# Optimization experiments

Measured on AMD Instinct MI355X. Metric: run time of the kernel, lower is better.

## Reference

```python
import jax, jax.numpy as jnp
import numpy as np

EPS = 1e-5

def conv2d(x, w, stride=1, pad=0, groups=1):
    return jax.lax.conv_general_dilated(
        x, w, (stride, stride), [(pad, pad), (pad, pad)],
        feature_group_count=groups,
        dimension_numbers=('NCHW', 'OIHW', 'NCHW'))

def prelu(x, a):
    return jnp.where(x > 0, x, a[None, :, None, None] * x)

def batchnorm(x, g, b):
    # training-mode BN: batch statistics over N,H,W (biased variance, as torch)
    m = jnp.mean(x, axis=(0, 2, 3), keepdims=True)
    v = jnp.var(x, axis=(0, 2, 3), keepdims=True)
    xhat = (x - m) * jax.lax.rsqrt(v + EPS)
    return xhat * g[None, :, None, None] + b[None, :, None, None]

def setup_inputs() -> dict:
    key = jax.random.key(0)
    ks = jax.random.split(key, 8)
    C_in, C_out, stride = 128, 256, 2
    x = jax.random.normal(ks[0], (32, C_in, 56, 56), dtype=jnp.float32)
    w1 = jax.random.normal(ks[1], (C_out, C_in, 1, 1), dtype=jnp.float32) * 0.05
    w_dw = jax.random.normal(ks[2], (C_out, 1, 3, 3), dtype=jnp.float32) * 0.1
    w3 = jax.random.normal(ks[3], (C_out, C_out, 1, 1), dtype=jnp.float32) * 0.05
    w_adj = jax.random.normal(ks[4], (C_out, C_in, 1, 1), dtype=jnp.float32) * 0.05
    a_init = jnp.full((C_out,), 0.25, dtype=jnp.float32)  # PReLU init
    ones = jnp.ones((C_out,), dtype=jnp.float32)
    zeros = jnp.zeros((C_out,), dtype=jnp.float32)
    return {
        'x': x,
        'w1': w1, 'a1': a_init, 'g1': ones, 'b1': zeros,
        'w_dw': w_dw, 'a2': a_init, 'g2': ones, 'b2': zeros,
        'w3': w3, 'a3': a_init, 'g3': ones, 'b3': zeros,
        'w_adj': w_adj,
    }

def reference(x, w1, a1, g1, b1, w_dw, a2, g2, b2, w3, a3, g3, b3, w_adj):
    stride, C_out = 2, w_dw.shape[0]
    residual = conv2d(x, w_adj, stride=stride)  # full-precision shortcut
    xs = jnp.sign(x)
    # binary 1x1 conv (sign(x) already signed; sign is idempotent)
    out = conv2d(jnp.sign(xs), jnp.sign(w1))
    out = batchnorm(prelu(out, a1), g1, b1)
    # binary depthwise 3x3, stride, pad 1
    out = conv2d(jnp.sign(out), jnp.sign(w_dw), stride=stride, pad=1, groups=C_out)
    out = batchnorm(prelu(out, a2), g2, b2)
    # binary 1x1 conv
    out = conv2d(jnp.sign(out), jnp.sign(w3))
    out = batchnorm(prelu(out, a3), g3, b3)
    return out + residual
```

## Files before the change

### kernel.cpp

```cpp
#include <hip/hip_runtime.h>
#include <stdint.h>

#define NB   32
#define CIN  128
#define COUT 256
#define HH   56
#define WW   56
#define S1   (HH*WW)
#define HO   28
#define WO   28
#define S2   (HO*WO)
#define NS1  (NB*S1)
#define NS2  (NB*S2)
#define TOT2 (NS2*COUT)
#define EPSV 1e-5f

constexpr size_t OFF_XBITS = 0;
constexpr size_t OFF_WB1   = OFF_XBITS + (size_t)NS1*8*4;
constexpr size_t OFF_WB3   = OFF_WB1 + 256*8*4;
constexpr size_t OFF_WDW   = OFF_WB3 + 256*16*4;
constexpr size_t OFF_ACC   = OFF_WDW + 4096;
constexpr size_t OFF_WBADJ = OFF_ACC + 3*256*4*sizeof(int);
constexpr size_t OFF_XG    = OFF_WBADJ + (size_t)COUT*CIN*2;
constexpr size_t OFF_OUT1  = OFF_XG + (size_t)NS2*CIN*2;
constexpr size_t OFF_OUT2  = OFF_OUT1 + (size_t)NS1*COUT;
constexpr size_t OFF_XB2   = OFF_OUT2 + (size_t)TOT2;
constexpr size_t OFF_OUT3  = OFF_XB2 + (size_t)NS2*16*4;

typedef __attribute__((ext_vector_type(8))) short bf16x8;
typedef __attribute__((ext_vector_type(4))) float f32x4;

__device__ __forceinline__ uint32_t f2bf(float v) {
  uint32_t u = __float_as_uint(v);
  return (u + 0x7fffu + ((u >> 16) & 1u)) >> 16;
}

__device__ __forceinline__ void bn_finalize(const int* __restrict__ acc4,
                                            float a, float g, float b, float inv_ns,
                                            float& sc, float& sh) {
  float ps = (float)acc4[0];
  float ng = (float)acc4[1];
  float pq = (float)acc4[2];
  float nq = (float)acc4[3];
  float mean = (ps + a*ng) * inv_ns;
  float ex2  = (pq + a*a*nq) * inv_ns;
  float var  = ex2 - mean*mean;
  float rs   = rsqrtf(var + EPSV);
  sc = rs * g;
  sh = b - mean * sc;
}

__global__ __launch_bounds__(256) void packx_kernel(
    const float* __restrict__ x, uint32_t* __restrict__ xbits,
    uint32_t* __restrict__ xg,
    const float* __restrict__ w1, const float* __restrict__ w3,
    const float* __restrict__ wdw, const float* __restrict__ wadj,
    uint32_t* __restrict__ wb1, uint32_t* __restrict__ wb3,
    int8_t* __restrict__ wdws, uint32_t* __restrict__ wbadj,
    int* __restrict__ accbase) {
  int wdx = blockIdx.y;
  if (wdx == 0 && blockIdx.x < 256 && threadIdx.x < 64) {
    int co = blockIdx.x;
    int l  = threadIdx.x;
    if (l < 12) {
      int set = l >> 2, k = l & 3;
      accbase[set*1024 + co*4 + k] = 0;
    }
    for (int h = 0; h < 2; ++h) {
      float v = w1[(size_t)co*CIN + h*64 + l];
      unsigned long long bp = __ballot(v > 0.f);
      unsigned long long bn = __ballot(v < 0.f);
      if (l == 0) {
        wb1[co*8 + 2*h    ] = (uint32_t)bp;
        wb1[co*8 + 2*h + 1] = (uint32_t)(bp >> 32);
        wb1[co*8 + 4 + 2*h    ] = (uint32_t)bn;
        wb1[co*8 + 4 + 2*h + 1] = (uint32_t)(bn >> 32);
      }
    }
    for (int h = 0; h < 4; ++h) {
      float v = w3[(size_t)co*COUT + h*64 + l];
      unsigned long long bp = __ballot(v > 0.f);
      unsigned long long bn = __ballot(v < 0.f);
      if (l == 0) {
        wb3[co*16 + 2*h    ] = (uint32_t)bp;
        wb3[co*16 + 2*h + 1] = (uint32_t)(bp >> 32);
        wb3[co*16 + 8 + 2*h    ] = (uint32_t)bn;
        wb3[co*16 + 8 + 2*h + 1] = (uint32_t)(bn >> 32);
      }
    }
    if (l < 9) {
      float v = wdw[co*9 + l];
      wdws[co*9 + l] = (int8_t)((v > 0.f) - (v < 0.f));
    }
    {
      float v0 = wadj[(size_t)co*CIN + 2*l];
      float v1 = wadj[(size_t)co*CIN + 2*l + 1];
      wbadj[co*64 + l] = f2bf(v0) | (f2bf(v1) << 16);
    }
  }

  int m = blockIdx.x*256 + threadIdx.x;
  int n = m / S1, hw = m % S1;
  size_t base = ((size_t)n*CIN + wdx*32)*S1 + hw;
  uint32_t p = 0, q = 0;
  uint32_t bv[16];
  #pragma unroll
  for (int j = 0; j < 32; ++j) {
    float v = x[base + (size_t)j*S1];
    p |= (uint32_t)(v > 0.f) << j;
    q |= (uint32_t)(v < 0.f) << j;
    uint32_t b = f2bf(v);
    if (j & 1) bv[j >> 1] |= b << 16; else bv[j >> 1] = b;
  }
  xbits[(size_t)m*8 + wdx    ] = p;
  xbits[(size_t)m*8 + 4 + wdx] = q;
  int h = hw / WW, w = hw % WW;
  if (((h | w) & 1) == 0) {
    int m2 = n*S2 + (h >> 1)*WO + (w >> 1);
    uint4* dst = (uint4*)(xg + (size_t)m2*64 + wdx*16);
    dst[0] = make_uint4(bv[0],  bv[1],  bv[2],  bv[3]);
    dst[1] = make_uint4(bv[4],  bv[5],  bv[6],  bv[7]);
    dst[2] = make_uint4(bv[8],  bv[9],  bv[10], bv[11]);
    dst[3] = make_uint4(bv[12], bv[13], bv[14], bv[15]);
  }
}

__global__ __launch_bounds__(256) void conv1_kernel(
    const uint32_t* __restrict__ xb, const uint32_t* __restrict__ wb,
    int8_t* __restrict__ out1) {
  int m = blockIdx.x*256 + threadIdx.x;
  int n = m / S1, hw = m % S1;
  const uint32_t* xw = xb + (size_t)m*8;
  uint32_t p0 = xw[0], p1 = xw[1], p2 = xw[2], p3 = xw[3];
  uint32_t q0 = xw[4], q1 = xw[5], q2 = xw[6], q3 = xw[7];
  int co0 = blockIdx.y * 32;
  size_t obase = ((size_t)n*COUT)*S1 + hw;
  bool nozero = (((p0|q0) & (p1|q1) & (p2|q2) & (p3|q3)) == 0xffffffffu);
  if (nozero) {
    #pragma unroll 4
    for (int co = co0; co < co0 + 32; ++co) {
      const uint32_t* w8 = wb + (size_t)co*8;
      int s = __popc(p0 ^ w8[0]) + __popc(p1 ^ w8[1])
            + __popc(p2 ^ w8[2]) + __popc(p3 ^ w8[3]);
      int acc = 128 - 2*s;
      if (acc > 127) acc = 127;
      out1[obase + (size_t)co*S1] = (int8_t)acc;
    }
  } else {
    #pragma unroll 4
    for (int co = co0; co < co0 + 32; ++co) {
      const uint32_t* w8 = wb + (size_t)co*8;
      uint32_t a0 = w8[0], a1 = w8[1], a2 = w8[2], a3 = w8[3];
      uint32_t b0 = w8[4], b1 = w8[5], b2 = w8[6], b3 = w8[7];
      int acc = __popc(p0&a0) + __popc(p1&a1) + __popc(p2&a2) + __popc(p3&a3)
              + __popc(q0&b0) + __popc(q1&b1) + __popc(q2&b2) + __popc(q3&b3)
              - __popc(p0&b0) - __popc(p1&b1) - __popc(p2&b2) - __popc(p3&b3)
              - __popc(q0&a0) - __popc(q1&a1) - __popc(q2&a2) - __popc(q3&a3);
      if (acc > 127) acc = 127;
      out1[obase + (size_t)co*S1] = (int8_t)acc;
    }
  }
}

__global__ __launch_bounds__(256) void stats_i8_kernel(
    const int8_t* __restrict__ buf, int* __restrict__ accum,
    int s_sp, int v16_per_block) {
  int co = blockIdx.x, slice = blockIdx.y;
  int base16 = slice * v16_per_block;
  int psum = 0, nsum = 0, psq = 0, nsq = 0;
  for (int i = threadIdx.x; i < v16_per_block; i += 256) {
    int flat = (base16 + i) * 16;
    int n = flat / s_sp, hw = flat % s_sp;
    int4 v = *reinterpret_cast<const int4*>(buf + (size_t)(n*COUT + co)*s_sp + hw);
    int ws[4] = {v.x, v.y, v.z, v.w};
    #pragma unroll
    for (int d = 0; d < 4; ++d) {
      #pragma unroll
      for (int k = 0; k < 4; ++k) {
        int f = (int)(int8_t)(ws[d] >> (8*k));
        if (f > 0) { psum += f; psq += f*f; } else { nsum += f; nsq += f*f; }
      }
    }
  }
  __shared__ int r0[256], r1[256], r2[256], r3[256];
  int t = threadIdx.x;
  r0[t] = psum; r1[t] = nsum; r2[t] = psq; r3[t] = nsq;
  __syncthreads();
  for (int s = 128; s > 0; s >>= 1) {
    if (t < s) { r0[t]+=r0[t+s]; r1[t]+=r1[t+s]; r2[t]+=r2[t+s]; r3[t]+=r3[t+s]; }
    __syncthreads();
  }
  if (t == 0) {
    atomicAdd(&accum[co*4+0], r0[0]);
    atomicAdd(&accum[co*4+1], r1[0]);
    atomicAdd(&accum[co*4+2], r2[0]);
    atomicAdd(&accum[co*4+3], r3[0]);
  }
}

__global__ __launch_bounds__(256) void stats_i16_kernel(
    const int16_t* __restrict__ buf, int* __restrict__ accum,
    int s_sp, int v8_per_block) {
  int co = blockIdx.x, slice = blockIdx.y;
  int base8 = slice * v8_per_block;
  int psum = 0, nsum = 0, psq = 0, nsq = 0;
  for (int i = threadIdx.x; i < v8_per_block; i += 256) {
    int flat = (base8 + i) * 8;
    int n = flat / s_sp, hw = flat % s_sp;
    int4 v = *reinterpret_cast<const int4*>(buf + (size_t)(n*COUT + co)*s_sp + hw);
    int ws[4] = {v.x, v.y, v.z, v.w};
    #pragma unroll
    for (int d = 0; d < 4; ++d) {
      int lo = (int)(short)(ws[d] & 0xffff);
      int hi = (int)(short)(ws[d] >> 16);
      if (lo > 0) { psum += lo; psq += lo*lo; } else { nsum += lo; nsq += lo*lo; }
      if (hi > 0) { psum += hi; psq += hi*hi; } else { nsum += hi; nsq += hi*hi; }
    }
  }
  __shared__ int r0[256], r1[256], r2[256], r3[256];
  int t = threadIdx.x;
  r0[t] = psum; r1[t] = nsum; r2[t] = psq; r3[t] = nsq;
  __syncthreads();
  for (int s = 128; s > 0; s >>= 1) {
    if (t < s) { r0[t]+=r0[t+s]; r1[t]+=r1[t+s]; r2[t]+=r2[t+s]; r3[t]+=r3[t+s]; }
    __syncthreads();
  }
  if (t == 0) {
    atomicAdd(&accum[co*4+0], r0[0]);
    atomicAdd(&accum[co*4+1], r1[0]);
    atomicAdd(&accum[co*4+2], r2[0]);
    atomicAdd(&accum[co*4+3], r3[0]);
  }
}

#define DW_SLABS 8
#define DW_RB    68
__global__ __launch_bounds__(256) void dw_kernel(
    const int8_t* __restrict__ out1, const int8_t* __restrict__ wdws,
    const int* __restrict__ acc1, const float* __restrict__ a1,
    const float* __restrict__ g1, const float* __restrict__ b1,
    int8_t* __restrict__ out2, int* __restrict__ accum2) {
  __shared__ int8_t sl[DW_SLABS][57][DW_RB];
  __shared__ int sTp[DW_SLABS], sTn[DW_SLABS], sAcc[DW_SLABS][4];
  int tid = threadIdx.x;
  int nc0 = blockIdx.x * DW_SLABS;
  int co0 = nc0 & (COUT-1);

  int* slw = (int*)&sl[0][0][0];
  #pragma unroll
  for (int i = tid; i < DW_SLABS*57*DW_RB/4; i += 256) slw[i] = 0;
  if (tid < DW_SLABS) { sTp[tid] = 128; sTn[tid] = -129; }
  if (tid < DW_SLABS*4) sAcc[tid >> 2][tid & 3] = 0;
  __syncthreads();

  {
    int slab = tid >> 5;
    int co = co0 + slab;
    float av = a1[co], sc, sh;
    bn_finalize(acc1 + co*4, av, g1[co], b1[co], 1.f/NS1, sc, sh);
    int tp = 128, tn = -129;
    int v0 = -128 + (tid & 31)*8;
    #pragma unroll
    for (int k = 0; k < 8; ++k) {
      int v = v0 + k;
      float f = (float)v;
      float pr = f > 0.f ? f : av*f;
      float tv = pr*sc + sh;
      if (tv > 0.f && v < tp) tp = v;
      if (tv < 0.f && v > tn) tn = v;
    }
    atomicMin(&sTp[slab], tp);
    atomicMax(&sTn[slab], tn);
  }
  __syncthreads();

  for (int i = tid; i < DW_SLABS*784; i += 256) {
    int slab = i / 784;
    int d    = i - slab*784;
    int ih   = d / 14;
    int iwd  = d - ih*14;
    int Tp = sTp[slab], Tn = sTn[slab];
    uint32_t v4 = ((const uint32_t*)(out1 + (size_t)(nc0 + slab)*S1))[d];
    uint32_t s4 = 0;
    #pragma unroll
    for (int k = 0; k < 4; ++k) {
      int v = (int)(int8_t)(v4 >> (8*k));
      int s = (v >= Tp) - (v <= Tn);
      s4 |= (uint32_t)(s & 0xff) << (8*k);
    }
    *(uint32_t*)&sl[slab][ih + 1][4 + 4*iwd] = s4;
  }
  __syncthreads();

  int psum = 0, nsum = 0, psq = 0, nsq = 0;
  int slabD = tid / HO;
  if (tid < DW_SLABS*HO) {
    int ho   = tid - slabD*HO;
    int nc = nc0 + slabD;
    int co = co0 + slabD;
    int wv[9];
    #pragma unroll
    for (int k = 0; k < 9; ++k) wv[k] = wdws[co*9 + k];
    const uint32_t* r0 = (const uint32_t*)&sl[slabD][2*ho    ][4];
    const uint32_t* r1 = (const uint32_t*)&sl[slabD][2*ho + 1][4];
    const uint32_t* r2 = (const uint32_t*)&sl[slabD][2*ho + 2][4];
    uint32_t* o32 = (uint32_t*)(out2 + (size_t)nc*S2 + ho*WO);
    int c0 = 0, c1 = 0, c2 = 0;
    uint32_t obuf = 0;
    #pragma unroll
    for (int q = 0; q < 14; ++q) {
      uint32_t d0 = r0[q], d1 = r1[q], d2 = r2[q];
      int s00=(int)(int8_t)d0, s01=(int)(int8_t)(d0>>8), s02=(int)(int8_t)(d0>>16), s03=(int)(int8_t)(d0>>24);
      int s10=(int)(int8_t)d1, s11=(int)(int8_t)(d1>>8), s12=(int)(int8_t)(d1>>16), s13=(int)(int8_t)(d1>>24);
      int s20=(int)(int8_t)d2, s21=(int)(int8_t)(d2>>8), s22=(int)(int8_t)(d2>>16), s23=(int)(int8_t)(d2>>24);
      int a0 = c0*wv[0] + s00*wv[1] + s01*wv[2]
             + c1*wv[3] + s10*wv[4] + s11*wv[5]
             + c2*wv[6] + s20*wv[7] + s21*wv[8];
      int a1v = s01*wv[0] + s02*wv[1] + s03*wv[2]
              + s11*wv[3] + s12*wv[4] + s13*wv[5]
              + s21*wv[6] + s22*wv[7] + s23*wv[8];
      c0 = s03; c1 = s13; c2 = s23;
      if (a0 > 0) { psum += a0; psq += a0*a0; } else { nsum += a0; nsq += a0*a0; }
      if (a1v > 0) { psum += a1v; psq += a1v*a1v; } else { nsum += a1v; nsq += a1v*a1v; }
      if ((q & 1) == 0) {
        obuf = (uint32_t)(a0 & 0xff) | ((uint32_t)(a1v & 0xff) << 8);
      } else {
        obuf |= ((uint32_t)(a0 & 0xff) << 16) | ((uint32_t)(a1v & 0xff) << 24);
        o32[q >> 1] = obuf;
      }
    }
    atomicAdd(&sAcc[slabD][0], psum);
    atomicAdd(&sAcc[slabD][1], nsum);
    atomicAdd(&sAcc[slabD][2], psq);
    atomicAdd(&sAcc[slabD][3], nsq);
  }
  __syncthreads();

  if (tid < DW_SLABS*4) {
    int slab = tid >> 2, k = tid & 3;
    atomicAdd(&accum2[(co0 + slab)*4 + k], sAcc[slab][k]);
  }
}

__global__ __launch_bounds__(256) void pack2_kernel(
    const int8_t* __restrict__ out2, const int* __restrict__ acc2,
    const float* __restrict__ a2, const float* __restrict__ g2,
    const float* __restrict__ b2, uint32_t* __restrict__ xb2) {
  __shared__ int sTp[32], sTn[32];
  int wdx = blockIdx.y;
  if (threadIdx.x < 32) {
    int c = wdx*32 + threadIdx.x;
    float av = a2[c], sc, sh;
    bn_finalize(acc2 + c*4, av, g2[c], b2[c], 1.f/NS2, sc, sh);
    int tp = 10, tn = -10;
    for (int v = -9; v <= 9; ++v) {
      float f = (float)v;
      float pr = f > 0.f ? f : av*f;
      float tv = pr*sc + sh;
      if (tv > 0.f && v < tp) tp = v;
      if (tv < 0.f && v > tn) tn = v;
    }
    sTp[threadIdx.x] = tp; sTn[threadIdx.x] = tn;
  }
  __syncthreads();
  int m = blockIdx.x*256 + threadIdx.x;
  int n = m / S2, hw = m % S2;
  uint32_t p = 0, q = 0;
  #pragma unroll
  for (int j = 0; j < 32; ++j) {
    int c = wdx*32 + j;
    int v = out2[(size_t)(n*COUT + c)*S2 + hw];
    p |= (uint32_t)(v >= sTp[j]) << j;
    q |= (uint32_t)(v <= sTn[j]) << j;
  }
  xb2[(size_t)m*16 + wdx    ] = p;
  xb2[(size_t)m*16 + 8 + wdx] = q;
}

__global__ __launch_bounds__(256) void conv3_kernel(
    const uint32_t* __restrict__ xb2, const uint32_t* __restrict__ wb3,
    int16_t* __restrict__ out3) {
  int m = blockIdx.x*256 + threadIdx.x;
  int n = m / S2, hw = m % S2;
  const uint32_t* xw = xb2 + (size_t)m*16;
  uint32_t P[8], Q[8];
  #pragma unroll
  for (int i = 0; i < 8; ++i) { P[i] = xw[i]; Q[i] = xw[8+i]; }
  int co0 = blockIdx.y * 32;
  size_t obase = ((size_t)n*COUT)*S2 + hw;
  uint32_t allm = 0xffffffffu;
  #pragma unroll
  for (int i = 0; i < 8; ++i) allm &= (P[i] | Q[i]);
  if (allm == 0xffffffffu) {
    #pragma unroll 2
    for (int co = co0; co < co0 + 32; ++co) {
      const uint32_t* w = wb3 + (size_t)co*16;
      int s = 0;
      #pragma unroll
      for (int i = 0; i < 8; ++i) s += __popc(P[i] ^ w[i]);
      out3[obase + (size_t)co*S2] = (int16_t)(256 - 2*s);
    }
  } else {
    #pragma unroll 2
    for (int co = co0; co < co0 + 32; ++co) {
      const uint32_t* w = wb3 + (size_t)co*16;
      int acc = 0;
      #pragma unroll
      for (int i = 0; i < 8; ++i) {
        uint32_t wp = w[i], wn = w[8+i];
        acc += __popc(P[i]&wp) + __popc(Q[i]&wn) - __popc(P[i]&wn) - __popc(Q[i]&wp);
      }
      out3[obase + (size_t)co*S2] = (int16_t)acc;
    }
  }
}

__global__ __launch_bounds__(256) void resfinal_kernel(
    const uint16_t* __restrict__ xg, const uint16_t* __restrict__ wb,
    const int16_t* __restrict__ out3,
    const float* __restrict__ a3, const float* __restrict__ g3,
    const float* __restrict__ b3, const int* __restrict__ acc3,
    float* __restrict__ out) {
  int lane = threadIdx.x & 63;
  int wid  = threadIdx.x >> 6;
  int m0  = blockIdx.x*64 + wid*16;
  int co0 = blockIdx.y*64;
  int r16 = lane & 15, hi = lane >> 4;
  int koff = hi * 8;

  const bf16x8* arow = (const bf16x8*)(xg + (size_t)(m0 + r16)*CIN + koff);
  bf16x8 af0 = arow[0], af1 = arow[4], af2 = arow[8], af3 = arow[12];

  f32x4 d0, d1, d2, d3;
  {
    const bf16x8* brow = (const bf16x8*)(wb + (size_t)(co0 + r16)*CIN + koff);
    f32x4 a = {0.f,0.f,0.f,0.f};
    a = __builtin_amdgcn_mfma_f32_16x16x32_bf16(af0, brow[0],  a, 0,0,0);
    a = __builtin_amdgcn_mfma_f32_16x16x32_bf16(af1, brow[4],  a, 0,0,0);
    a = __builtin_amdgcn_mfma_f32_16x16x32_bf16(af2, brow[8],  a, 0,0,0);
    a = __builtin_amdgcn_mfma_f32_16x16x32_bf16(af3, brow[12], a, 0,0,0);
    d0 = a;
  }
  {
    const bf16x8* brow = (const bf16x8*)(wb + (size_t)(co0 + 16 + r16)*CIN + koff);
    f32x4 a = {0.f,0.f,0.f,0.f};
    a = __builtin_amdgcn_mfma_f32_16x16x32_bf16(af0, brow[0],  a, 0,0,0);
    a = __builtin_amdgcn_mfma_f32_16x16x32_bf16(af1, brow[4],  a, 0,0,0);
    a = __builtin_amdgcn_mfma_f32_16x16x32_bf16(af2, brow[8],  a, 0,0,0);
    a = __builtin_amdgcn_mfma_f32_16x16x32_bf16(af3, brow[12], a, 0,0,0);
    d1 = a;
  }
  {
    const bf16x8* brow = (const bf16x8*)(wb + (size_t)(co0 + 32 + r16)*CIN + koff);
    f32x4 a = {0.f,0.f,0.f,0.f};
    a = __builtin_amdgcn_mfma_f32_16x16x32_bf16(af0, brow[0],  a, 0,0,0);
    a = __builtin_amdgcn_mfma_f32_16x16x32_bf16(af1, brow[4],  a, 0,0,0);
    a = __builtin_amdgcn_mfma_f32_16x16x32_bf16(af2, brow[8],  a, 0,0,0);
    a = __builtin_amdgcn_mfma_f32_16x16x32_bf16(af3, brow[12], a, 0,0,0);
    d2 = a;
  }
  {
    const bf16x8* brow = (const bf16x8*)(wb + (size_t)(co0 + 48 + r16)*CIN + koff);
    f32x4 a = {0.f,0.f,0.f,0.f};
    a = __builtin_amdgcn_mfma_f32_16x16x32_bf16(af0, brow[0],  a, 0,0,0);
    a = __builtin_amdgcn_mfma_f32_16x16x32_bf16(af1, brow[4],  a, 0,0,0);
    a = __builtin_amdgcn_mfma_f32_16x16x32_bf16(af2, brow[8],  a, 0,0,0);
    a = __builtin_amdgcn_mfma_f32_16x16x32_bf16(af3, brow[12], a, 0,0,0);
    d3 = a;
  }

  int mrow = m0 + hi*4;
  int n  = mrow / S2;
  int hw = mrow - n*S2;
  f32x4 dd[4] = {d0, d1, d2, d3};
  #pragma unroll
  for (int t = 0; t < 4; ++t) {
    int co = co0 + t*16 + r16;
    float av = a3[co], sc, sh;
    bn_finalize(acc3 + co*4, av, g3[co], b3[co], 1.f/NS2, sc, sh);
    size_t o = ((size_t)n*COUT + co)*S2 + hw;
    #pragma unroll
    for (int r = 0; r < 4; ++r) {
      float f = (float)out3[o + r];
      float pp = f > 0.f ? f : av*f;
      out[o + r] = pp*sc + sh + dd[t][r];
    }
  }
}

extern "C" void kernel_launch(void* const* d_in, const int* in_sizes, int n_in,
                              void* d_out, int out_size, void* d_ws, size_t ws_size,
                              hipStream_t stream) {
  (void)in_sizes; (void)n_in; (void)out_size; (void)ws_size;
  const float* x    = (const float*)d_in[0];
  const float* w1   = (const float*)d_in[1];
  const float* a1   = (const float*)d_in[2];
  const float* g1   = (const float*)d_in[3];
  const float* b1   = (const float*)d_in[4];
  const float* wdw  = (const float*)d_in[5];
  const float* a2   = (const float*)d_in[6];
  const float* g2   = (const float*)d_in[7];
  const float* b2   = (const float*)d_in[8];
  const float* w3   = (const float*)d_in[9];
  const float* a3   = (const float*)d_in[10];
  const float* g3   = (const float*)d_in[11];
  const float* b3   = (const float*)d_in[12];
  const float* wadj = (const float*)d_in[13];
  float* out = (float*)d_out;

  char* ws = (char*)d_ws;
  uint32_t* xbits = (uint32_t*)(ws + OFF_XBITS);
  uint32_t* wb1   = (uint32_t*)(ws + OFF_WB1);
  uint32_t* wb3   = (uint32_t*)(ws + OFF_WB3);
  int8_t*   wdws  = (int8_t*)  (ws + OFF_WDW);
  int*      acc1  = (int*)     (ws + OFF_ACC);
  int*      acc2  = acc1 + 256*4;
  int*      acc3  = acc2 + 256*4;
  uint32_t* wbadj = (uint32_t*)(ws + OFF_WBADJ);
  uint32_t* xg    = (uint32_t*)(ws + OFF_XG);
  int8_t*   out1  = (int8_t*)  (ws + OFF_OUT1);
  int8_t*   out2  = (int8_t*)  (ws + OFF_OUT2);
  uint32_t* xb2   = (uint32_t*)(ws + OFF_XB2);
  int16_t*  out3  = (int16_t*) (ws + OFF_OUT3);

  packx_kernel<<<dim3(NS1/256, 4), 256, 0, stream>>>(
      x, xbits, xg, w1, w3, wdw, wadj, wb1, wb3, wdws, wbadj, acc1);
  conv1_kernel<<<dim3(NS1/256, 8), 256, 0, stream>>>(xbits, wb1, out1);
  stats_i8_kernel<<<dim3(256, 4), 256, 0, stream>>>(out1, acc1, S1, 1568);
  dw_kernel<<<NB*COUT/DW_SLABS, 256, 0, stream>>>(out1, wdws, acc1, a1, g1, b1, out2, acc2);
  pack2_kernel<<<dim3(NS2/256, 8), 256, 0, stream>>>(out2, acc2, a2, g2, b2, xb2);
  conv3_kernel<<<dim3(NS2/256, 8), 256, 0, stream>>>(xb2, wb3, out3);
  stats_i16_kernel<<<dim3(256, 4), 256, 0, stream>>>(out3, acc3, S2, 784);
  resfinal_kernel<<<dim3(NS2/64, COUT/64), 256, 0, stream>>>(
      (const uint16_t*)xg, (const uint16_t*)wbadj, out3, a3, g3, b3, acc3, out);
}
```

Measured before the change: 110.0 us.

## Fuse BN statistics into conv1 and conv3 and widen resfinal blocks

The separate int8 and int16 BN-statistics kernels are removed. conv1 and conv3 now keep their 32 per-thread outputs in registers, transpose them through shared memory, reduce per-channel positive and negative sums and squares with shuffles, and atomically add them to the accumulators. This avoids re-reading out1 and out3 from global memory and saves two launches, at the cost of many more atomics (one set per block per channel). resfinal now computes all 256 output channels per block with 16 MFMA tiles instead of 64, which raises register pressure but reuses the A fragments and cuts the grid size.

```diff
diff --git a/kernel.cpp b/kernel.cpp
--- a/kernel.cpp
+++ b/kernel.cpp
@@ -127,29 +127,31 @@
 
 __global__ __launch_bounds__(256) void conv1_kernel(
     const uint32_t* __restrict__ xb, const uint32_t* __restrict__ wb,
-    int8_t* __restrict__ out1) {
-  int m = blockIdx.x*256 + threadIdx.x;
+    int8_t* __restrict__ out1, int* __restrict__ accum1) {
+  int tid = threadIdx.x;
+  int m = blockIdx.x*256 + tid;
   int n = m / S1, hw = m % S1;
   const uint32_t* xw = xb + (size_t)m*8;
   uint32_t p0 = xw[0], p1 = xw[1], p2 = xw[2], p3 = xw[3];
   uint32_t q0 = xw[4], q1 = xw[5], q2 = xw[6], q3 = xw[7];
   int co0 = blockIdx.y * 32;
   size_t obase = ((size_t)n*COUT)*S1 + hw;
+  int8_t a8[32];
   bool nozero = (((p0|q0) & (p1|q1) & (p2|q2) & (p3|q3)) == 0xffffffffu);
   if (nozero) {
     #pragma unroll 4
-    for (int co = co0; co < co0 + 32; ++co) {
-      const uint32_t* w8 = wb + (size_t)co*8;
+    for (int j = 0; j < 32; ++j) {
+      const uint32_t* w8 = wb + (size_t)(co0 + j)*8;
       int s = __popc(p0 ^ w8[0]) + __popc(p1 ^ w8[1])
             + __popc(p2 ^ w8[2]) + __popc(p3 ^ w8[3]);
       int acc = 128 - 2*s;
       if (acc > 127) acc = 127;
-      out1[obase + (size_t)co*S1] = (int8_t)acc;
+      a8[j] = (int8_t)acc;
     }
   } else {
     #pragma unroll 4
-    for (int co = co0; co < co0 + 32; ++co) {
-      const uint32_t* w8 = wb + (size_t)co*8;
+    for (int j = 0; j < 32; ++j) {
+      const uint32_t* w8 = wb + (size_t)(co0 + j)*8;
       uint32_t a0 = w8[0], a1 = w8[1], a2 = w8[2], a3 = w8[3];
       uint32_t b0 = w8[4], b1 = w8[5], b2 = w8[6], b3 = w8[7];
       int acc = __popc(p0&a0) + __popc(p1&a1) + __popc(p2&a2) + __popc(p3&a3)
@@ -157,79 +159,42 @@
               - __popc(p0&b0) - __popc(p1&b1) - __popc(p2&b2) - __popc(p3&b3)
               - __popc(q0&a0) - __popc(q1&a1) - __popc(q2&a2) - __popc(q3&a3);
       if (acc > 127) acc = 127;
-      out1[obase + (size_t)co*S1] = (int8_t)acc;
-    }
-  }
-}
-
-__global__ __launch_bounds__(256) void stats_i8_kernel(
-    const int8_t* __restrict__ buf, int* __restrict__ accum,
-    int s_sp, int v16_per_block) {
-  int co = blockIdx.x, slice = blockIdx.y;
-  int base16 = slice * v16_per_block;
-  int psum = 0, nsum = 0, psq = 0, nsq = 0;
-  for (int i = threadIdx.x; i < v16_per_block; i += 256) {
-    int flat = (base16 + i) * 16;
-    int n = flat / s_sp, hw = flat % s_sp;
-    int4 v = *reinterpret_cast<const int4*>(buf + (size_t)(n*COUT + co)*s_sp + hw);
-    int ws[4] = {v.x, v.y, v.z, v.w};
-    #pragma unroll
-    for (int d = 0; d < 4; ++d) {
-      #pragma unroll
-      for (int k = 0; k < 4; ++k) {
-        int f = (int)(int8_t)(ws[d] >> (8*k));
-        if (f > 0) { psum += f; psq += f*f; } else { nsum += f; nsq += f*f; }
-      }
-    }
-  }
-  __shared__ int r0[256], r1[256], r2[256], r3[256];
-  int t = threadIdx.x;
-  r0[t] = psum; r1[t] = nsum; r2[t] = psq; r3[t] = nsq;
-  __syncthreads();
-  for (int s = 128; s > 0; s >>= 1) {
-    if (t < s) { r0[t]+=r0[t+s]; r1[t]+=r1[t+s]; r2[t]+=r2[t+s]; r3[t]+=r3[t+s]; }
-    __syncthreads();
-  }
-  if (t == 0) {
-    atomicAdd(&accum[co*4+0], r0[0]);
-    atomicAdd(&accum[co*4+1], r1[0]);
-    atomicAdd(&accum[co*4+2], r2[0]);
-    atomicAdd(&accum[co*4+3], r3[0]);
-  }
-}
-
-__global__ __launch_bounds__(256) void stats_i16_kernel(
-    const int16_t* __restrict__ buf, int* __restrict__ accum,
-    int s_sp, int v8_per_block) {
-  int co = blockIdx.x, slice = blockIdx.y;
-  int base8 = slice * v8_per_block;
-  int psum = 0, nsum = 0, psq = 0, nsq = 0;
-  for (int i = threadIdx.x; i < v8_per_block; i += 256) {
-    int flat = (base8 + i) * 8;
-    int n = flat / s_sp, hw = flat % s_sp;
-    int4 v = *reinterpret_cast<const int4*>(buf + (size_t)(n*COUT + co)*s_sp + hw);
-    int ws[4] = {v.x, v.y, v.z, v.w};
-    #pragma unroll
-    for (int d = 0; d < 4; ++d) {
-      int lo = (int)(short)(ws[d] & 0xffff);
-      int hi = (int)(short)(ws[d] >> 16);
-      if (lo > 0) { psum += lo; psq += lo*lo; } else { nsum += lo; nsq += lo*lo; }
-      if (hi > 0) { psum += hi; psq += hi*hi; } else { nsum += hi; nsq += hi*hi; }
-    }
-  }
-  __shared__ int r0[256], r1[256], r2[256], r3[256];
-  int t = threadIdx.x;
-  r0[t] = psum; r1[t] = nsum; r2[t] = psq; r3[t] = nsq;
-  __syncthreads();
-  for (int s = 128; s > 0; s >>= 1) {
-    if (t < s) { r0[t]+=r0[t+s]; r1[t]+=r1[t+s]; r2[t]+=r2[t+s]; r3[t]+=r3[t+s]; }
-    __syncthreads();
-  }
-  if (t == 0) {
-    atomicAdd(&accum[co*4+0], r0[0]);
-    atomicAdd(&accum[co*4+1], r1[0]);
-    atomicAdd(&accum[co*4+2], r2[0]);
-    atomicAdd(&accum[co*4+3], r3[0]);
+      a8[j] = (int8_t)acc;
+    }
+  }
+  #pragma unroll 8
+  for (int j = 0; j < 32; ++j) out1[obase + (size_t)(co0 + j)*S1] = a8[j];
+
+  __shared__ int8_t vals[256][36];
+  #pragma unroll
+  for (int k = 0; k < 8; ++k) {
+    uint32_t w4 = (uint32_t)(uint8_t)a8[4*k]
+                | ((uint32_t)(uint8_t)a8[4*k+1] << 8)
+                | ((uint32_t)(uint8_t)a8[4*k+2] << 16)
+                | ((uint32_t)(uint8_t)a8[4*k+3] << 24);
+    *(uint32_t*)&vals[tid][4*k] = w4;
+  }
+  __syncthreads();
+  int j = tid >> 3;
+  int c = tid & 7;
+  int ps = 0, ns = 0, pq = 0, nq = 0;
+  #pragma unroll
+  for (int i = 0; i < 32; ++i) {
+    int v = (int)vals[c*32 + i][j];
+    if (v > 0) { ps += v; pq += v*v; } else { ns += v; nq += v*v; }
+  }
+  #pragma unroll
+  for (int off = 4; off; off >>= 1) {
+    ps += __shfl_xor(ps, off);
+    ns += __shfl_xor(ns, off);
+    pq += __shfl_xor(pq, off);
+    nq += __shfl_xor(nq, off);
+  }
+  if (c == 0) {
+    atomicAdd(&accum1[(co0 + j)*4 + 0], ps);
+    atomicAdd(&accum1[(co0 + j)*4 + 1], ns);
+    atomicAdd(&accum1[(co0 + j)*4 + 2], pq);
+    atomicAdd(&accum1[(co0 + j)*4 + 3], nq);
   }
 }
 
@@ -379,8 +344,9 @@
 
 __global__ __launch_bounds__(256) void conv3_kernel(
     const uint32_t* __restrict__ xb2, const uint32_t* __restrict__ wb3,
-    int16_t* __restrict__ out3) {
-  int m = blockIdx.x*256 + threadIdx.x;
+    int16_t* __restrict__ out3, int* __restrict__ accum3) {
+  int tid = threadIdx.x;
+  int m = blockIdx.x*256 + tid;
   int n = m / S2, hw = m % S2;
   const uint32_t* xw = xb2 + (size_t)m*16;
   uint32_t P[8], Q[8];
@@ -388,30 +354,62 @@
   for (int i = 0; i < 8; ++i) { P[i] = xw[i]; Q[i] = xw[8+i]; }
   int co0 = blockIdx.y * 32;
   size_t obase = ((size_t)n*COUT)*S2 + hw;
+  int16_t a16[32];
   uint32_t allm = 0xffffffffu;
   #pragma unroll
   for (int i = 0; i < 8; ++i) allm &= (P[i] | Q[i]);
   if (allm == 0xffffffffu) {
     #pragma unroll 2
-    for (int co = co0; co < co0 + 32; ++co) {
-      const uint32_t* w = wb3 + (size_t)co*16;
+    for (int j = 0; j < 32; ++j) {
+      const uint32_t* w = wb3 + (size_t)(co0 + j)*16;
       int s = 0;
       #pragma unroll
       for (int i = 0; i < 8; ++i) s += __popc(P[i] ^ w[i]);
-      out3[obase + (size_t)co*S2] = (int16_t)(256 - 2*s);
+      a16[j] = (int16_t)(256 - 2*s);
     }
   } else {
     #pragma unroll 2
-    for (int co = co0; co < co0 + 32; ++co) {
-      const uint32_t* w = wb3 + (size_t)co*16;
+    for (int j = 0; j < 32; ++j) {
+      const uint32_t* w = wb3 + (size_t)(co0 + j)*16;
       int acc = 0;
       #pragma unroll
       for (int i = 0; i < 8; ++i) {
         uint32_t wp = w[i], wn = w[8+i];
         acc += __popc(P[i]&wp) + __popc(Q[i]&wn) - __popc(P[i]&wn) - __popc(Q[i]&wp);
       }
-      out3[obase + (size_t)co*S2] = (int16_t)acc;
-    }
+      a16[j] = (int16_t)acc;
+    }
+  }
+  #pragma unroll 8
+  for (int j = 0; j < 32; ++j) out3[obase + (size_t)(co0 + j)*S2] = a16[j];
+
+  __shared__ int16_t vals[256][34];
+  #pragma unroll
+  for (int k = 0; k < 16; ++k) {
+    uint32_t w2 = (uint32_t)(uint16_t)a16[2*k] | ((uint32_t)(uint16_t)a16[2*k+1] << 16);
+    *(uint32_t*)&vals[tid][2*k] = w2;
+  }
+  __syncthreads();
+  int j = tid >> 3;
+  int c = tid & 7;
+  int ps = 0, ns = 0, pq = 0, nq = 0;
+  #pragma unroll
+  for (int i = 0; i < 32; ++i) {
+    int v = (int)vals[c*32 + i][j];
+    if (v > 0) { ps += v; pq += v*v; } else { ns += v; nq += v*v; }
+  }
+  #pragma unroll
+  for (int off = 4; off; off >>= 1) {
+    ps += __shfl_xor(ps, off);
+    ns += __shfl_xor(ns, off);
+    pq += __shfl_xor(pq, off);
+    nq += __shfl_xor(nq, off);
+  }
+  if (c == 0) {
+    atomicAdd(&accum3[(co0 + j)*4 + 0], ps);
+    atomicAdd(&accum3[(co0 + j)*4 + 1], ns);
+    atomicAdd(&accum3[(co0 + j)*4 + 2], pq);
+    atomicAdd(&accum3[(co0 + j)*4 + 3], nq);
   }
 }
 
@@ -424,58 +422,30 @@
   int lane = threadIdx.x & 63;
   int wid  = threadIdx.x >> 6;
   int m0  = blockIdx.x*64 + wid*16;
-  int co0 = blockIdx.y*64;
   int r16 = lane & 15, hi = lane >> 4;
   int koff = hi * 8;
 
   const bf16x8* arow = (const bf16x8*)(xg + (size_t)(m0 + r16)*CIN + koff);
   bf16x8 af0 = arow[0], af1 = arow[4], af2 = arow[8], af3 = arow[12];
 
-  f32x4 d0, d1, d2, d3;
-  {
-    const bf16x8* brow = (const bf16x8*)(wb + (size_t)(co0 + r16)*CIN + koff);
+  f32x4 dd[16];
+  #pragma unroll
+  for (int t = 0; t < 16; ++t) {
+    const bf16x8* brow = (const bf16x8*)(wb + (size_t)(t*16 + r16)*CIN + koff);
     f32x4 a = {0.f,0.f,0.f,0.f};
     a = __builtin_amdgcn_mfma_f32_16x16x32_bf16(af0, brow[0],  a, 0,0,0);
     a = __builtin_amdgcn_mfma_f32_16x16x32_bf16(af1, brow[4],  a, 0,0,0);
     a = __builtin_amdgcn_mfma_f32_16x16x32_bf16(af2, brow[8],  a, 0,0,0);
     a = __builtin_amdgcn_mfma_f32_16x16x32_bf16(af3, brow[12], a, 0,0,0);
-    d0 = a;
-  }
-  {
-    const bf16x8* brow = (const bf16x8*)(wb + (size_t)(co0 + 16 + r16)*CIN + koff);
-    f32x4 a = {0.f,0.f,0.f,0.f};
-    a = __builtin_amdgcn_mfma_f32_16x16x32_bf16(af0, brow[0],  a, 0,0,0);
-    a = __builtin_amdgcn_mfma_f32_16x16x32_bf16(af1, brow[4],  a, 0,0,0);
-    a = __builtin_amdgcn_mfma_f32_16x16x32_bf16(af2, brow[8],  a, 0,0,0);
-    a = __builtin_amdgcn_mfma_f32_16x16x32_bf16(af3, brow[12], a, 0,0,0);
-    d1 = a;
-  }
-  {
-    const bf16x8* brow = (const bf16x8*)(wb + (size_t)(co0 + 32 + r16)*CIN + koff);
-    f32x4 a = {0.f,0.f,0.f,0.f};
-    a = __builtin_amdgcn_mfma_f32_16x16x32_bf16(af0, brow[0],  a, 0,0,0);
-    a = __builtin_amdgcn_mfma_f32_16x16x32_bf16(af1, brow[4],  a, 0,0,0);
-    a = __builtin_amdgcn_mfma_f32_16x16x32_bf16(af2, brow[8],  a, 0,0,0);
-    a = __builtin_amdgcn_mfma_f32_16x16x32_bf16(af3, brow[12], a, 0,0,0);
-    d2 = a;
-  }
-  {
-    const bf16x8* brow = (const bf16x8*)(wb + (size_t)(co0 + 48 + r16)*CIN + koff);
-    f32x4 a = {0.f,0.f,0.f,0.f};
-    a = __builtin_amdgcn_mfma_f32_16x16x32_bf16(af0, brow[0],  a, 0,0,0);
-    a = __builtin_amdgcn_mfma_f32_16x16x32_bf16(af1, brow[4],  a, 0,0,0);
-    a = __builtin_amdgcn_mfma_f32_16x16x32_bf16(af2, brow[8],  a, 0,0,0);
-    a = __builtin_amdgcn_mfma_f32_16x16x32_bf16(af3, brow[12], a, 0,0,0);
-    d3 = a;
+    dd[t] = a;
   }
 
   int mrow = m0 + hi*4;
   int n  = mrow / S2;
   int hw = mrow - n*S2;
-  f32x4 dd[4] = {d0, d1, d2, d3};
-  #pragma unroll
-  for (int t = 0; t < 4; ++t) {
-    int co = co0 + t*16 + r16;
+  #pragma unroll
+  for (int t = 0; t < 16; ++t) {
+    int co = t*16 + r16;
     float av = a3[co], sc, sh;
     bn_finalize(acc3 + co*4, av, g3[co], b3[co], 1.f/NS2, sc, sh);
     size_t o = ((size_t)n*COUT + co)*S2 + hw;
@@ -525,12 +495,10 @@
 
   packx_kernel<<<dim3(NS1/256, 4), 256, 0, stream>>>(
       x, xbits, xg, w1, w3, wdw, wadj, wb1, wb3, wdws, wbadj, acc1);
-  conv1_kernel<<<dim3(NS1/256, 8), 256, 0, stream>>>(xbits, wb1, out1);
-  stats_i8_kernel<<<dim3(256, 4), 256, 0, stream>>>(out1, acc1, S1, 1568);
+  conv1_kernel<<<dim3(NS1/256, 8), 256, 0, stream>>>(xbits, wb1, out1, acc1);
   dw_kernel<<<NB*COUT/DW_SLABS, 256, 0, stream>>>(out1, wdws, acc1, a1, g1, b1, out2, acc2);
   pack2_kernel<<<dim3(NS2/256, 8), 256, 0, stream>>>(out2, acc2, a2, g2, b2, xb2);
-  conv3_kernel<<<dim3(NS2/256, 8), 256, 0, stream>>>(xb2, wb3, out3);
-  stats_i16_kernel<<<dim3(256, 4), 256, 0, stream>>>(out3, acc3, S2, 784);
-  resfinal_kernel<<<dim3(NS2/64, COUT/64), 256, 0, stream>>>(
+  conv3_kernel<<<dim3(NS2/256, 8), 256, 0, stream>>>(xb2, wb3, out3, acc3);
+  resfinal_kernel<<<NS2/64, 256, 0, stream>>>(
       (const uint16_t*)xg, (const uint16_t*)wbadj, out3, a3, g3, b3, acc3, out);
 }
```

New measurement: 325.1 us. +195.6%, slower.
